# Kernel tuning notes

Hardware: AMD Instinct MI355X
Metric: run time of the kernel (lower is better)

Reference implementation:

```python
import jax, jax.numpy as jnp
import numpy as np

EPS = 1e-5
SLOPE = 0.2


def _conv(x, w, b, stride, pad):
    y = jax.lax.conv_general_dilated(
        x, w, (stride, stride), ((pad, pad), (pad, pad)),
        dimension_numbers=('NCHW', 'OIHW', 'NCHW'))
    return y + b[None, :, None, None]


def _inorm(x):
    m = x.mean(axis=(2, 3), keepdims=True)
    v = x.var(axis=(2, 3), keepdims=True)
    return (x - m) * jax.lax.rsqrt(v + EPS)


def _down(x, w, b, norm):
    y = _conv(x, w, b, 2, 1)
    if norm:
        y = _inorm(y)
    return jax.nn.leaky_relu(y, SLOPE)


def _self_attn(x, wq, bq, wk, bk, wv, bv, gamma):
    B, C, H, W = x.shape
    N = H * W
    q = _conv(x, wq, bq, 1, 0).reshape(B, -1, N)   # (B, C/8, N)
    k = _conv(x, wk, bk, 1, 0).reshape(B, -1, N)
    v = _conv(x, wv, bv, 1, 0).reshape(B, C, N)
    attn = jax.nn.softmax(jnp.einsum('bcn,bcm->bnm', q, k), axis=-1)  # (B,N,N)
    out = jnp.einsum('bcm,bnm->bcn', v, attn).reshape(B, C, H, W)
    return gamma * out + x


def _branch(p, img):
    (w0, b0, w1, b1, w2, b2, wq, bq, wk, bk, wv, bv, gamma, wh, bh) = p
    x = _down(img, w0, b0, norm=False)
    x = _down(x, w1, b1, norm=True)
    x = _self_attn(x, wq, bq, wk, bk, wv, bv, gamma)
    x = _down(x, w2, b2, norm=True)
    return _conv(x, wh, bh, 1, 1)  # head: Conv2d(nf*4, 1, 4, padding=1)


def setup_inputs() -> dict:
    key = jax.random.key(0)
    ks = jax.random.split(key, 20)
    S, B, H = 4, 16, 128
    s = 0.05  # weight scale for numerical stability of softmax energies
    d = {
        'img': jax.random.normal(ks[0], (B, 1, H, H), jnp.float32),
        'stage_idx': jax.random.randint(ks[1], (B,), 0, S, jnp.int32),
        'w0': jax.random.normal(ks[2], (S, 64, 1, 4, 4)) * s,
        'b0': jax.random.normal(ks[3], (S, 64)) * s,
        'w1': jax.random.normal(ks[4], (S, 128, 64, 4, 4)) * s,
        'b1': jax.random.normal(ks[5], (S, 128)) * s,
        'w2': jax.random.normal(ks[6], (S, 256, 128, 4, 4)) * s,
        'b2': jax.random.normal(ks[7], (S, 256)) * s,
        'wq': jax.random.normal(ks[8], (S, 16, 128, 1, 1)) * s,
        'bq': jax.random.normal(ks[9], (S, 16)) * s,
        'wk': jax.random.normal(ks[10], (S, 16, 128, 1, 1)) * s,
        'bk': jax.random.normal(ks[11], (S, 16)) * s,
        'wv': jax.random.normal(ks[12], (S, 128, 128, 1, 1)) * s,
        'bv': jax.random.normal(ks[13], (S, 128)) * s,
        'gamma': jax.random.normal(ks[14], (S,)) * s,
        'wh': jax.random.normal(ks[15], (S, 1, 256, 4, 4)) * s,
        'bh': jax.random.normal(ks[16], (S, 1)) * s,
    }
    return d


def reference(img, stage_idx, w0, b0, w1, b1, w2, b2, wq, bq, wk, bk, wv, bv, gamma, wh, bh):
    params = (w0, b0, w1, b1, w2, b2, wq, bq, wk, bk, wv, bv, gamma, wh, bh)
    # compute every branch for every sample (as the original), stacked over stage axis
    all_preds = jax.vmap(_branch, in_axes=(0, None))(params, img)  # (S, B, 1, h, w)
    B = img.shape[0]
    return all_preds[stage_idx, jnp.arange(B)]  # (B, 1, h, w)
```

## Files before the change

kernel.cpp:

```cpp
#include <hip/hip_runtime.h>

#define LRELU(x) ((x) > 0.0f ? (x) : 0.2f * (x))
#define SB __builtin_amdgcn_sched_barrier(0)

typedef short bf16x8 __attribute__((ext_vector_type(8)));
typedef short bf16x4 __attribute__((ext_vector_type(4)));
typedef float f32x4 __attribute__((ext_vector_type(4)));

__device__ __forceinline__ short f2bf(float f) {
  union { float f; unsigned u; } x{f};
  return (short)((x.u + 0x7FFF + ((x.u >> 16) & 1)) >> 16);
}

__global__ __launch_bounds__(256) void k_repack_all(
    const float* __restrict__ w1, unsigned short* __restrict__ wr1,
    const float* __restrict__ w2, unsigned short* __restrict__ wr2,
    const float* __restrict__ bh, const int* __restrict__ sidx,
    float* __restrict__ out, unsigned short* __restrict__ x0t,
    unsigned short* __restrict__ ybf, const float* __restrict__ img,
    const float* __restrict__ w0, const float* __restrict__ b0,
    float* __restrict__ stat) {
  __shared__ float Ish[4 * 34];
  if (blockIdx.x >= 2853) {
    const int t = threadIdx.x;
    const int q = blockIdx.x - 2853;
    const int b = q >> 8, py = q & 255;
    const int oh = py >> 2, owb = (py & 3) << 4;
    const int s = sidx[b];
    const float* ip = img + (size_t)b * 16384;
    if (t < 136) {
      int r = t / 34, c = t % 34;
      int ih = 2 * oh - 1 + r, iw = 2 * owb - 1 + c;
      Ish[t] = ((unsigned)ih < 128u && (unsigned)iw < 128u) ? ip[ih * 128 + iw] : 0.f;
    }
    const int co = t & 63, ps = t >> 6;
    float wreg[16];
    const float* wp = w0 + (s * 64 + co) * 16;
#pragma unroll
    for (int i = 0; i < 16; i++) wreg[i] = wp[i];
    float bb = b0[s * 64 + co];
    __syncthreads();
    unsigned short* op = x0t + ((size_t)b * 4356 + (oh + 1) * 66 + (owb + 1)) * 64 + co;
#pragma unroll
    for (int j = 0; j < 4; j++) {
      int pl = ps * 4 + j;
      float acc = bb;
#pragma unroll
      for (int kh = 0; kh < 4; kh++)
#pragma unroll
        for (int kw = 0; kw < 4; kw++)
          acc += wreg[kh * 4 + kw] * Ish[kh * 34 + pl * 2 + kw];
      acc = LRELU(acc);
      op[pl * 64] = (unsigned short)f2bf(acc);
    }
    return;
  }
  int idx = blockIdx.x * 256 + threadIdx.x;
  if (idx < 131072) {
    float4 v = *(const float4*)(w1 + (size_t)idx * 4);
    int base = idx * 4;
    int tap0 = base & 15;
    int rest = base >> 4;
    int ci = rest & 63, sco = rest >> 6;
    unsigned short* d = wr1 + (size_t)sco * 1024 + ci;
    d[(tap0 + 0) * 64] = (unsigned short)f2bf(v.x);
    d[(tap0 + 1) * 64] = (unsigned short)f2bf(v.y);
    d[(tap0 + 2) * 64] = (unsigned short)f2bf(v.z);
    d[(tap0 + 3) * 64] = (unsigned short)f2bf(v.w);
    return;
  } else if (idx < 655360) {
    int i = idx - 131072;
    float4 v = *(const float4*)(w2 + (size_t)i * 4);
    int base = i * 4;
    int tap0 = base & 15;
    int rest = base >> 4;
    int ci = rest & 127, sco = rest >> 7;
    unsigned short* d = wr2 + (size_t)sco * 2048 + ci;
    d[(tap0 + 0) * 128] = (unsigned short)f2bf(v.x);
    d[(tap0 + 1) * 128] = (unsigned short)f2bf(v.y);
    d[(tap0 + 2) * 128] = (unsigned short)f2bf(v.z);
    d[(tap0 + 3) * 128] = (unsigned short)f2bf(v.w);
    return;
  } else if (idx < 658960) {
    int i = idx - 655360;
    if (i < 3600) out[i] = bh[sidx[i / 225]];
    return;
  } else if (idx < 692240) {
    int i = idx - 658960;
    int b = i / 2080, r = i % 2080;
    int pix = r >> 3, sub = r & 7;
    int row, col;
    if (pix < 66) { row = 0; col = pix; }
    else if (pix < 132) { row = 65; col = pix - 66; }
    else { int qq = pix - 132; row = 1 + (qq >> 1); col = (qq & 1) * 65; }
    bf16x8 z = {0, 0, 0, 0, 0, 0, 0, 0};
    *(bf16x8*)(x0t + ((size_t)b * 4356 + row * 66 + col) * 64 + sub * 8) = z;
    return;
  } else if (idx < 726032) {
    int i = idx - 692240;
    if (i >= 33792) return;
    int b = i / 2112, r = i % 2112;
    int pix = r >> 4, sub = r & 15;
    int row, col;
    if (pix < 34) { row = 0; col = pix; }
    else if (pix < 68) { row = 33; col = pix - 34; }
    else { int qq = pix - 68; row = 1 + (qq >> 1); col = (qq & 1) * 33; }
    bf16x8 z = {0, 0, 0, 0, 0, 0, 0, 0};
    *(bf16x8*)(ybf + ((size_t)b * 1156 + row * 34 + col) * 128 + sub * 8) = z;
    return;
  } else {
    int i = idx - 726032;
    if (i < 4096) stat[i] = 0.f;
    return;
  }
}

__global__ __launch_bounds__(256, 2) void k_conv1n(
    const unsigned short* __restrict__ x0t, const unsigned short* __restrict__ wr,
    const int* __restrict__ sidx, float* __restrict__ x1,
    float* __restrict__ stat) {
  __shared__ __align__(16) unsigned short Xs[26624];
  const int t = threadIdx.x;
  const int c = blockIdx.x & 7, rr = blockIdx.x >> 3;
  const int b = c + 8 * (rr >> 5);
  const int y = rr & 31;
  const int ne = y & 15;
  const int cog = y >> 4;
  const int s = sidx[b];
  const int lane = t & 63, wv = t >> 6;
  const int quad = lane >> 4, l16 = lane & 15;

  const unsigned short* gb = x0t + ((size_t)b * 4356 + 4 * ne * 66) * 64;
  {
    float4 v[13];
#pragma unroll
    for (int i = 0; i < 13; i++) v[i] = *(const float4*)(gb + (i * 256 + t) * 8);
#pragma unroll
    for (int i = 0; i < 13; i++) {
      int ba = (i * 256 + t) * 16;
      int sw = ba ^ (((ba >> 9) & 7) << 4);
      *(float4*)((char*)Xs + sw) = v[i];
    }
  }
  __syncthreads();

  const int co0w = cog * 64 + wv * 16;
  const unsigned short* ap = wr + ((size_t)(s * 128 + co0w + l16)) * 1024 + quad * 8;
  f32x4 acc[4];
#pragma unroll
  for (int nt = 0; nt < 4; nt++) acc[nt] = (f32x4){0.f, 0.f, 0.f, 0.f};

#pragma unroll
  for (int kc = 0; kc < 32; kc++) {
    const int tap = kc >> 1;
    const int cio = (kc & 1) * 32 + quad * 8;
    const int kh = tap >> 2, kw = tap & 3;
    bf16x8 af = *(const bf16x8*)(ap + kc * 32);
#pragma unroll
    for (int nt = 0; nt < 4; nt++) {
      int lr = 2 * (nt >> 1) + kh;
      int col = 2 * ((nt & 1) * 16 + l16) + kw;
      int ba = ((lr * 66 + col) * 64 + cio) * 2;
      int sw = ba ^ (((ba >> 9) & 7) << 4);
      bf16x8 bv = *(const bf16x8*)((const char*)Xs + sw);
      acc[nt] = __builtin_amdgcn_mfma_f32_16x16x32_bf16(af, bv, acc[nt], 0, 0, 0);
    }
  }

#pragma unroll
  for (int r = 0; r < 4; r++) {
    float sv = acc[0][r] + acc[1][r] + acc[2][r] + acc[3][r];
    float sq = acc[0][r] * acc[0][r] + acc[1][r] * acc[1][r] +
               acc[2][r] * acc[2][r] + acc[3][r] * acc[3][r];
#pragma unroll
    for (int o = 1; o < 16; o <<= 1) {
      sv += __shfl_xor(sv, o, 64);
      sq += __shfl_xor(sq, o, 64);
    }
    if (l16 == 0) {
      int co = co0w + quad * 4 + r;
      atomicAdd(&stat[(b * 128 + co) * 2 + 0], sv);
      atomicAdd(&stat[(b * 128 + co) * 2 + 1], sq);
    }
  }

#pragma unroll
  for (int nt = 0; nt < 4; nt++) {
    int p = ne * 64 + (nt >> 1) * 32 + (nt & 1) * 16 + l16;
#pragma unroll
    for (int r = 0; r < 4; r++)
      x1[((size_t)b * 128 + co0w + quad * 4 + r) * 1024 + p] = acc[nt][r];
  }
}

__global__ __launch_bounds__(256) void k_proj_qkv(
    const float* __restrict__ xin, const float* __restrict__ wq,
    const float* __restrict__ bq, const float* __restrict__ wk,
    const float* __restrict__ bk, const float* __restrict__ wv,
    const float* __restrict__ bv, const int* __restrict__ sidx,
    const float* __restrict__ stat,
    float* __restrict__ q, float* __restrict__ kout, unsigned short* __restrict__ vpk) {
  __shared__ float xsh[32 * 256];
  __shared__ float wsh[16 * 32];
  __shared__ float msh[128], ish[128];
  const int t = threadIdx.x;
  const int c = blockIdx.x & 7, rr = blockIdx.x >> 3;
  const int half = (rr >= 40) ? 1 : 0;
  const int b = c + 8 * half;
  const int y = rr - half * 40;
  const int s = sidx[b];
  const int cg = t >> 6, ng = t & 63;
  const float* w;
  const float* bias;
  int co0, nn0, CO;
  if (y < 8) {
    w = (y < 4) ? wq : wk;
    bias = (y < 4) ? bq : bk;
    co0 = 0;
    nn0 = (y & 3) * 256;
    CO = 16;
  } else {
    w = wv;
    bias = bv;
    co0 = ((y - 8) >> 2) * 16;
    nn0 = ((y - 8) & 3) * 256;
    CO = 128;
  }
  if (t < 128) {
    float sv = stat[(b * 128 + t) * 2 + 0];
    float sq = stat[(b * 128 + t) * 2 + 1];
    float m = sv * (1.0f / 1024.0f);
    float var = sq * (1.0f / 1024.0f) - m * m;
    msh[t] = m;
    ish[t] = rsqrtf(var + 1e-5f);
  }
  const float* xb = xin + (size_t)b * 128 * 1024;
  float4 acc4[4];
#pragma unroll
  for (int cix = 0; cix < 4; cix++) {
    float bb = bias[s * CO + co0 + cg * 4 + cix];
    acc4[cix] = make_float4(bb, bb, bb, bb);
  }
  __syncthreads();
  for (int cc = 0; cc < 4; cc++) {
#pragma unroll
    for (int k = 0; k < 8; k++) {
      int id = t + (k << 8);
      int ci = id >> 6, nf = id & 63;
      float4 v = ((const float4*)(xb + (cc * 32 + ci) * 1024 + nn0))[nf];
      float m = msh[cc * 32 + ci], iv = ish[cc * 32 + ci];
      v.x = (v.x - m) * iv; v.x = LRELU(v.x);
      v.y = (v.y - m) * iv; v.y = LRELU(v.y);
      v.z = (v.z - m) * iv; v.z = LRELU(v.z);
      v.w = (v.w - m) * iv; v.w = LRELU(v.w);
      ((float4*)xsh)[id] = v;
    }
    if (t < 128)
      ((float4*)wsh)[t] =
          ((const float4*)(w + ((size_t)(s * CO + co0 + (t >> 3))) * 128 + cc * 32))[t & 7];
    __syncthreads();
#pragma unroll
    for (int ci4 = 0; ci4 < 8; ci4++) {
      float4 wvv[4], xv[4];
#pragma unroll
      for (int cix = 0; cix < 4; cix++) wvv[cix] = ((const float4*)wsh)[(cg * 4 + cix) * 8 + ci4];
#pragma unroll
      for (int i = 0; i < 4; i++) xv[i] = ((const float4*)xsh)[(ci4 * 4 + i) * 64 + ng];
#pragma unroll
      for (int cix = 0; cix < 4; cix++)
#pragma unroll
        for (int i = 0; i < 4; i++) {
          float wvc = i == 0 ? wvv[cix].x : i == 1 ? wvv[cix].y : i == 2 ? wvv[cix].z : wvv[cix].w;
          acc4[cix].x += wvc * xv[i].x;
          acc4[cix].y += wvc * xv[i].y;
          acc4[cix].z += wvc * xv[i].z;
          acc4[cix].w += wvc * xv[i].w;
        }
    }
    __syncthreads();
  }
  if (y < 8) {
    float* outp = (y < 4) ? q : kout;
#pragma unroll
    for (int cix = 0; cix < 4; cix++)
      ((float4*)(outp + ((size_t)b * 16 + cg * 4 + cix) * 1024 + nn0))[ng] = acc4[cix];
  } else {
    int n = nn0 + ng * 4;
#pragma unroll
    for (int cix = 0; cix < 4; cix++) {
      int co = co0 + cg * 4 + cix;
      bf16x4 u;
      u[0] = f2bf(acc4[cix].x);
      u[1] = f2bf(acc4[cix].y);
      u[2] = f2bf(acc4[cix].z);
      u[3] = f2bf(acc4[cix].w);
      *(bf16x4*)(vpk + (((size_t)b * 32 + (n >> 5)) * 128 + co) * 32 + (n & 31)) = u;
    }
  }
}

__global__ __launch_bounds__(256, 2) void k_attn(
    const float* __restrict__ q, const float* __restrict__ k,
    const unsigned short* __restrict__ vpk, const float* __restrict__ x1,
    const float* __restrict__ gamma, const int* __restrict__ sidx,
    const float* __restrict__ stat, unsigned short* __restrict__ ybf) {
  __shared__ __align__(16) short Psh[16 * 1032];
  __shared__ __align__(16) unsigned short Ks[16384];
  __shared__ float redm[64], reds[64];
  const int t = threadIdx.x;
  const int c = blockIdx.x & 7, rr = blockIdx.x >> 3;
  const int b = c + 8 * (rr >> 6);
  const int n0 = (rr & 63) << 4;
  const int lane = t & 63, wv = t >> 6;
  const int quad = lane >> 4, l16 = lane & 15;
  const float* qb = q + (size_t)b * 16 * 1024;
  const float* kb = k + (size_t)b * 16 * 1024;
  const float* xb = x1 + (size_t)b * 128 * 1024;

  bf16x8 qf = {0, 0, 0, 0, 0, 0, 0, 0};
  if (quad < 2) {
#pragma unroll
    for (int i = 0; i < 8; i++)
      qf[i] = f2bf(qb[(size_t)(quad * 8 + i) * 1024 + n0 + l16]);
  }

#pragma unroll
  for (int cg = 0; cg < 4; cg++) {
    float4 v0 = *(const float4*)(kb + (size_t)(cg * 4 + 0) * 1024 + 4 * t);
    float4 v1 = *(const float4*)(kb + (size_t)(cg * 4 + 1) * 1024 + 4 * t);
    float4 v2 = *(const float4*)(kb + (size_t)(cg * 4 + 2) * 1024 + 4 * t);
    float4 v3 = *(const float4*)(kb + (size_t)(cg * 4 + 3) * 1024 + 4 * t);
#pragma unroll
    for (int j = 0; j < 4; j++) {
      float a0 = j == 0 ? v0.x : j == 1 ? v0.y : j == 2 ? v0.z : v0.w;
      float a1 = j == 0 ? v1.x : j == 1 ? v1.y : j == 2 ? v1.z : v1.w;
      float a2 = j == 0 ? v2.x : j == 1 ? v2.y : j == 2 ? v2.z : v2.w;
      float a3 = j == 0 ? v3.x : j == 1 ? v3.y : j == 2 ? v3.z : v3.w;
      bf16x4 pk;
      pk[0] = f2bf(a0);
      pk[1] = f2bf(a1);
      pk[2] = f2bf(a2);
      pk[3] = f2bf(a3);
      *(bf16x4*)&Ks[(4 * t + j) * 16 + cg * 4] = pk;
    }
  }
  __syncthreads();

  f32x4 sacc[16];
#pragma unroll
  for (int tt = 0; tt < 16; tt++) sacc[tt] = (f32x4){0.f, 0.f, 0.f, 0.f};
  const int mwb = wv * 256;
#pragma unroll
  for (int tt = 0; tt < 16; tt++) {
    bf16x8 afr = {0, 0, 0, 0, 0, 0, 0, 0};
    if (quad < 2)
      afr = *(const bf16x8*)&Ks[(mwb + tt * 16 + l16) * 16 + quad * 8];
    sacc[tt] = __builtin_amdgcn_mfma_f32_16x16x32_bf16(afr, qf, sacc[tt], 0, 0, 0);
  }

  float lmax = sacc[0][0];
#pragma unroll
  for (int tt = 0; tt < 16; tt++)
#pragma unroll
    for (int r = 0; r < 4; r++) lmax = fmaxf(lmax, sacc[tt][r]);
  lmax = fmaxf(lmax, __shfl_xor(lmax, 16, 64));
  lmax = fmaxf(lmax, __shfl_xor(lmax, 32, 64));
  if (lane < 16) redm[wv * 16 + lane] = lmax;
  __syncthreads();
  float gmax = fmaxf(fmaxf(redm[l16], redm[16 + l16]), fmaxf(redm[32 + l16], redm[48 + l16]));

  float lsum = 0.f;
#pragma unroll
  for (int tt = 0; tt < 16; tt++) {
    bf16x4 pv4;
#pragma unroll
    for (int r = 0; r < 4; r++) {
      float e = __expf(sacc[tt][r] - gmax);
      lsum += e;
      pv4[r] = f2bf(e);
    }
    *(bf16x4*)&Psh[l16 * 1032 + mwb + tt * 16 + quad * 4] = pv4;
  }
  lsum += __shfl_xor(lsum, 16, 64);
  lsum += __shfl_xor(lsum, 32, 64);
  if (lane < 16) reds[wv * 16 + lane] = lsum;
  __syncthreads();

  const unsigned short* vp =
      vpk + ((size_t)b * 32 * 128 + (size_t)(wv * 32 + l16)) * 32 + quad * 8;
  const short* prow = Psh + l16 * 1032 + quad * 8;
  f32x4 dacc[2];
  dacc[0] = (f32x4){0.f, 0.f, 0.f, 0.f};
  dacc[1] = (f32x4){0.f, 0.f, 0.f, 0.f};

  bf16x8 VA0[4], VA1[4], PAr[4];
  bf16x8 VB0[4], VB1[4], PBr[4];
#define LDV(V0, V1, PR, G)                                \
  _Pragma("unroll") for (int m4 = 0; m4 < 4; m4++) {      \
    int mt = (G) * 4 + m4;                                \
    V0[m4] = *(const bf16x8*)(vp + mt * 4096);            \
    V1[m4] = *(const bf16x8*)(vp + 512 + mt * 4096);      \
    PR[m4] = *(const bf16x8*)(prow + mt * 32);            \
  }                                                       \
  SB;
#define MMV(V0, V1, PR)                                                                      \
  _Pragma("unroll") for (int m4 = 0; m4 < 4; m4++) {                                         \
    dacc[0] = __builtin_amdgcn_mfma_f32_16x16x32_bf16(V0[m4], PR[m4], dacc[0], 0, 0, 0);     \
    dacc[1] = __builtin_amdgcn_mfma_f32_16x16x32_bf16(V1[m4], PR[m4], dacc[1], 0, 0, 0);     \
  }                                                                                          \
  SB;

  LDV(VA0, VA1, PAr, 0)
  LDV(VB0, VB1, PBr, 1)
  MMV(VA0, VA1, PAr) LDV(VA0, VA1, PAr, 2)
  MMV(VB0, VB1, PBr) LDV(VB0, VB1, PBr, 3)
  MMV(VA0, VA1, PAr) LDV(VA0, VA1, PAr, 4)
  MMV(VB0, VB1, PBr) LDV(VB0, VB1, PBr, 5)
  MMV(VA0, VA1, PAr) LDV(VA0, VA1, PAr, 6)
  MMV(VB0, VB1, PBr) LDV(VB0, VB1, PBr, 7)
  MMV(VA0, VA1, PAr)
  MMV(VB0, VB1, PBr)
#undef LDV
#undef MMV
  __syncthreads();

  float* Osh = (float*)Psh;
  short* Osh2 = Psh + 4352;
#pragma unroll
  for (int i = 0; i < 2; i++) {
    int cob = wv * 32 + i * 16 + quad * 4;
#pragma unroll
    for (int r = 0; r < 4; r++) Osh[(cob + r) * 17 + l16] = dacc[i][r];
  }
  __syncthreads();
  float g = gamma[sidx[b]];
  {
    int co = t >> 1, j0 = (t & 1) * 8;
    float sv = stat[(b * 128 + co) * 2 + 0];
    float sq = stat[(b * 128 + co) * 2 + 1];
    float mm = sv * (1.0f / 1024.0f);
    float iv = rsqrtf(sq * (1.0f / 1024.0f) - mm * mm + 1e-5f);
    const float* xr = xb + (co << 10) + n0 + j0;
    float4 xv0 = *(const float4*)xr;
    float4 xv1 = *(const float4*)(xr + 4);
    float xs[8] = {xv0.x, xv0.y, xv0.z, xv0.w, xv1.x, xv1.y, xv1.z, xv1.w};
#pragma unroll
    for (int j = 0; j < 8; j++) {
      float nv = (xs[j] - mm) * iv;
      xs[j] = LRELU(nv);
    }
#pragma unroll
    for (int j = 0; j < 8; j++) {
      int nl = j0 + j;
      float rs = 1.0f / (reds[nl] + reds[16 + nl] + reds[32 + nl] + reds[48 + nl]);
      Osh2[nl * 136 + co] = f2bf(g * Osh[co * 17 + nl] * rs + xs[j]);
    }
  }
  __syncthreads();
  {
    int nl = t >> 4, cg = t & 15;
    bf16x8 u = *(const bf16x8*)&Osh2[nl * 136 + cg * 8];
    int p = n0 + nl;
    int ih = p >> 5, iw = p & 31;
    *(bf16x8*)(ybf + ((size_t)b * 1156 + (ih + 1) * 34 + (iw + 1)) * 128 + cg * 8) = u;
  }
}

__global__ __launch_bounds__(256, 2) void k_conv2n(
    const unsigned short* __restrict__ ybf, const unsigned short* __restrict__ wr,
    const int* __restrict__ sidx, float* __restrict__ x2) {
  __shared__ __align__(16) unsigned short Xs[26624];
  const int t = threadIdx.x;
  const int c = blockIdx.x & 7, rr = blockIdx.x >> 3;
  const int b = c + 8 * (rr >> 5);
  const int y = rr & 31;
  const int ne = y & 7;
  const int cog = y >> 3;
  const int s = sidx[b];
  const int lane = t & 63, wv = t >> 6;
  const int quad = lane >> 4, l16 = lane & 15;

  const unsigned short* gb = ybf + ((size_t)b * 1156 + 4 * ne * 34) * 128;
  {
    float4 v[13];
#pragma unroll
    for (int i = 0; i < 13; i++) v[i] = *(const float4*)(gb + (i * 256 + t) * 8);
#pragma unroll
    for (int i = 0; i < 13; i++) {
      int ba = (i * 256 + t) * 16;
      int sw = ba ^ (((ba >> 9) & 7) << 4);
      *(float4*)((char*)Xs + sw) = v[i];
    }
  }
  __syncthreads();

  const int co0w = cog * 64 + wv * 16;
  const unsigned short* ap = wr + ((size_t)(s * 256 + co0w + l16)) * 2048 + quad * 8;
  f32x4 acc[2];
  acc[0] = (f32x4){0.f, 0.f, 0.f, 0.f};
  acc[1] = (f32x4){0.f, 0.f, 0.f, 0.f};

#pragma unroll
  for (int kc = 0; kc < 64; kc++) {
    const int tap = kc >> 2;
    const int cio = (kc & 3) * 32 + quad * 8;
    const int kh = tap >> 2, kw = tap & 3;
    bf16x8 af = *(const bf16x8*)(ap + kc * 32);
#pragma unroll
    for (int nt = 0; nt < 2; nt++) {
      int lr = 2 * nt + kh;
      int col = 2 * l16 + kw;
      int ba = ((lr * 34 + col) * 128 + cio) * 2;
      int sw = ba ^ (((ba >> 9) & 7) << 4);
      bf16x8 bv = *(const bf16x8*)((const char*)Xs + sw);
      acc[nt] = __builtin_amdgcn_mfma_f32_16x16x32_bf16(af, bv, acc[nt], 0, 0, 0);
    }
  }

#pragma unroll
  for (int nt = 0; nt < 2; nt++) {
    int p = ne * 32 + nt * 16 + l16;
#pragma unroll
    for (int r = 0; r < 4; r++)
      x2[((size_t)b * 256 + co0w + quad * 4 + r) * 256 + p] = acc[nt][r];
  }
}

__global__ __launch_bounds__(256) void k_head_part(
    const float* __restrict__ x2, const float* __restrict__ wh,
    const int* __restrict__ sidx, float* __restrict__ out) {
  __shared__ float Xs[32 * 256];
  __shared__ float Wsh[512];
  __shared__ float sm[32], si[32];
  const int t = threadIdx.x;
  const int b = blockIdx.x, cc = blockIdx.y;
  const int s = sidx[b];
  const float* xp = x2 + ((size_t)b * 256 + cc * 32) * 256;
#pragma unroll
  for (int i = 0; i < 32; i++) Xs[i * 256 + t] = xp[i * 256 + t];
#pragma unroll
  for (int i = 0; i < 2; i++) {
    int idx = i * 256 + t;
    Wsh[idx] = wh[s * 4096 + cc * 512 + idx];
  }
  __syncthreads();
  {
    int r = t >> 3, c0 = (t & 7) * 32;
    float sv = 0.f, sq = 0.f;
#pragma unroll
    for (int j = 0; j < 32; j++) {
      float v = Xs[r * 256 + c0 + j];
      sv += v;
      sq += v * v;
    }
#pragma unroll
    for (int o = 1; o < 8; o <<= 1) {
      sv += __shfl_xor(sv, o, 64);
      sq += __shfl_xor(sq, o, 64);
    }
    if ((t & 7) == 0) {
      float m = sv * (1.0f / 256.0f);
      float var = sq * (1.0f / 256.0f) - m * m;
      sm[r] = m;
      si[r] = rsqrtf(var + 1e-5f);
    }
  }
  __syncthreads();
#pragma unroll
  for (int i = 0; i < 32; i++) {
    float v = (Xs[i * 256 + t] - sm[i]) * si[i];
    Xs[i * 256 + t] = LRELU(v);
  }
  __syncthreads();
  if (t < 225) {
    int oh = t / 15, ow = t % 15;
    float acc = 0.0f;
    for (int ci = 0; ci < 32; ci++) {
      const float* xr = Xs + ci * 256;
      const float* wr = Wsh + ci * 16;
#pragma unroll
      for (int kh = 0; kh < 4; kh++) {
        int ih = oh - 1 + kh;
        if ((unsigned)ih >= 16u) continue;
#pragma unroll
        for (int kw = 0; kw < 4; kw++) {
          int iw = ow - 1 + kw;
          if ((unsigned)iw >= 16u) continue;
          acc += wr[kh * 4 + kw] * xr[(ih << 4) + iw];
        }
      }
    }
    atomicAdd(out + b * 225 + t, acc);
  }
}

extern "C" void kernel_launch(void* const* d_in, const int* in_sizes, int n_in,
                              void* d_out, int out_size, void* d_ws, size_t ws_size,
                              hipStream_t stream) {
  const float* img = (const float*)d_in[0];
  const int* sidx = (const int*)d_in[1];
  const float* w0 = (const float*)d_in[2];
  const float* b0 = (const float*)d_in[3];
  const float* w1 = (const float*)d_in[4];
  const float* w2 = (const float*)d_in[6];
  const float* wq = (const float*)d_in[8];
  const float* bq = (const float*)d_in[9];
  const float* wk = (const float*)d_in[10];
  const float* bk = (const float*)d_in[11];
  const float* wv = (const float*)d_in[12];
  const float* bv = (const float*)d_in[13];
  const float* gamma = (const float*)d_in[14];
  const float* wh = (const float*)d_in[15];
  const float* bh = (const float*)d_in[16];
  float* out = (float*)d_out;

  float* ws = (float*)d_ws;
  unsigned short* x0t = (unsigned short*)(ws);
  float* x1 = ws + 2359296;
  float* q = ws + 4456448;
  float* k = ws + 4718592;
  unsigned short* vpk = (unsigned short*)(ws + 4980736);
  unsigned short* ybf = (unsigned short*)(ws + 6029312);
  float* x2 = ws + 7340032;
  float* stat = ws + 8650752;
  unsigned short* wr1 = (unsigned short*)(ws + 8912896);
  unsigned short* wr2 = (unsigned short*)(ws + 9175040);

  k_repack_all<<<6949, 256, 0, stream>>>(w1, wr1, w2, wr2, bh, sidx, out, x0t, ybf,
                                         img, w0, b0, stat);
  k_conv1n<<<512, 256, 0, stream>>>(x0t, wr1, sidx, x1, stat);
  k_proj_qkv<<<640, 256, 0, stream>>>(x1, wq, bq, wk, bk, wv, bv, sidx, stat, q, k, vpk);
  k_attn<<<1024, 256, 0, stream>>>(q, k, vpk, x1, gamma, sidx, stat, ybf);
  k_conv2n<<<512, 256, 0, stream>>>(ybf, wr2, sidx, x2);
  k_head_part<<<dim3(16, 8), 256, 0, stream>>>(x2, wh, sidx, out);
}
```

Before: 200.3 us.

## Emit Q/K as bf16 position-major from projection and load MFMA fragments directly

The projection kernel now writes Q and K as bf16 in a position-major [n][16] layout instead of fp32 channel-major. The attention kernel no longer loads all of K, converts it and stages it in shared memory behind a barrier. It reads MFMA fragments for Q and K straight from global memory. This halves Q/K traffic, removes the per-block conversion work and 32KB of LDS (which may allow more occupancy), but K fragments are now fetched from global or L2 rather than LDS.

Result: no change. 197.8 us (-1.2%).

```diff
diff --git a/kernel.cpp b/kernel.cpp
--- a/kernel.cpp
+++ b/kernel.cpp
@@ -199,7 +199,8 @@
     const float* __restrict__ bk, const float* __restrict__ wv,
     const float* __restrict__ bv, const int* __restrict__ sidx,
     const float* __restrict__ stat,
-    float* __restrict__ q, float* __restrict__ kout, unsigned short* __restrict__ vpk) {
+    unsigned short* __restrict__ qbf, unsigned short* __restrict__ kbf,
+    unsigned short* __restrict__ vpk) {
   __shared__ float xsh[32 * 256];
   __shared__ float wsh[16 * 32];
   __shared__ float msh[128], ish[128];
@@ -280,10 +281,18 @@
     __syncthreads();
   }
   if (y < 8) {
-    float* outp = (y < 4) ? q : kout;
-#pragma unroll
-    for (int cix = 0; cix < 4; cix++)
-      ((float4*)(outp + ((size_t)b * 16 + cg * 4 + cix) * 1024 + nn0))[ng] = acc4[cix];
+    unsigned short* outp = ((y < 4) ? qbf : kbf) + (size_t)b * 16384;
+#pragma unroll
+    for (int j = 0; j < 4; j++) {
+      bf16x4 u;
+#pragma unroll
+      for (int cix = 0; cix < 4; cix++) {
+        float v = j == 0 ? acc4[cix].x : j == 1 ? acc4[cix].y : j == 2 ? acc4[cix].z
+                                                                       : acc4[cix].w;
+        u[cix] = f2bf(v);
+      }
+      *(bf16x4*)(outp + (size_t)(nn0 + ng * 4 + j) * 16 + cg * 4) = u;
+    }
   } else {
     int n = nn0 + ng * 4;
 #pragma unroll
@@ -300,12 +309,11 @@
 }
 
 __global__ __launch_bounds__(256, 2) void k_attn(
-    const float* __restrict__ q, const float* __restrict__ k,
+    const unsigned short* __restrict__ qbf, const unsigned short* __restrict__ kbf,
     const unsigned short* __restrict__ vpk, const float* __restrict__ x1,
     const float* __restrict__ gamma, const int* __restrict__ sidx,
     const float* __restrict__ stat, unsigned short* __restrict__ ybf) {
   __shared__ __align__(16) short Psh[16 * 1032];
-  __shared__ __align__(16) unsigned short Ks[16384];
   __shared__ float redm[64], reds[64];
   const int t = threadIdx.x;
   const int c = blockIdx.x & 7, rr = blockIdx.x >> 3;
@@ -313,38 +321,12 @@
   const int n0 = (rr & 63) << 4;
   const int lane = t & 63, wv = t >> 6;
   const int quad = lane >> 4, l16 = lane & 15;
-  const float* qb = q + (size_t)b * 16 * 1024;
-  const float* kb = k + (size_t)b * 16 * 1024;
+  const unsigned short* qbb = qbf + (size_t)b * 16384;
+  const unsigned short* kbb = kbf + (size_t)b * 16384;
   const float* xb = x1 + (size_t)b * 128 * 1024;
 
   bf16x8 qf = {0, 0, 0, 0, 0, 0, 0, 0};
-  if (quad < 2) {
-#pragma unroll
-    for (int i = 0; i < 8; i++)
-      qf[i] = f2bf(qb[(size_t)(quad * 8 + i) * 1024 + n0 + l16]);
-  }
-
-#pragma unroll
-  for (int cg = 0; cg < 4; cg++) {
-    float4 v0 = *(const float4*)(kb + (size_t)(cg * 4 + 0) * 1024 + 4 * t);
-    float4 v1 = *(const float4*)(kb + (size_t)(cg * 4 + 1) * 1024 + 4 * t);
-    float4 v2 = *(const float4*)(kb + (size_t)(cg * 4 + 2) * 1024 + 4 * t);
-    float4 v3 = *(const float4*)(kb + (size_t)(cg * 4 + 3) * 1024 + 4 * t);
-#pragma unroll
-    for (int j = 0; j < 4; j++) {
-      float a0 = j == 0 ? v0.x : j == 1 ? v0.y : j == 2 ? v0.z : v0.w;
-      float a1 = j == 0 ? v1.x : j == 1 ? v1.y : j == 2 ? v1.z : v1.w;
-      float a2 = j == 0 ? v2.x : j == 1 ? v2.y : j == 2 ? v2.z : v2.w;
-      float a3 = j == 0 ? v3.x : j == 1 ? v3.y : j == 2 ? v3.z : v3.w;
-      bf16x4 pk;
-      pk[0] = f2bf(a0);
-      pk[1] = f2bf(a1);
-      pk[2] = f2bf(a2);
-      pk[3] = f2bf(a3);
-      *(bf16x4*)&Ks[(4 * t + j) * 16 + cg * 4] = pk;
-    }
-  }
-  __syncthreads();
+  if (quad < 2) qf = *(const bf16x8*)(qbb + (size_t)(n0 + l16) * 16 + quad * 8);
 
   f32x4 sacc[16];
 #pragma unroll
@@ -354,7 +336,7 @@
   for (int tt = 0; tt < 16; tt++) {
     bf16x8 afr = {0, 0, 0, 0, 0, 0, 0, 0};
     if (quad < 2)
-      afr = *(const bf16x8*)&Ks[(mwb + tt * 16 + l16) * 16 + quad * 8];
+      afr = *(const bf16x8*)(kbb + (size_t)(mwb + tt * 16 + l16) * 16 + quad * 8);
     sacc[tt] = __builtin_amdgcn_mfma_f32_16x16x32_bf16(afr, qf, sacc[tt], 0, 0, 0);
   }
 
@@ -617,8 +599,8 @@
   float* ws = (float*)d_ws;
   unsigned short* x0t = (unsigned short*)(ws);
   float* x1 = ws + 2359296;
-  float* q = ws + 4456448;
-  float* k = ws + 4718592;
+  unsigned short* qbf = (unsigned short*)(ws + 4456448);
+  unsigned short* kbf = (unsigned short*)(ws + 4718592);
   unsigned short* vpk = (unsigned short*)(ws + 4980736);
   unsigned short* ybf = (unsigned short*)(ws + 6029312);
   float* x2 = ws + 7340032;
@@ -629,8 +611,8 @@
   k_repack_all<<<6949, 256, 0, stream>>>(w1, wr1, w2, wr2, bh, sidx, out, x0t, ybf,
                                          img, w0, b0, stat);
   k_conv1n<<<512, 256, 0, stream>>>(x0t, wr1, sidx, x1, stat);
-  k_proj_qkv<<<640, 256, 0, stream>>>(x1, wq, bq, wk, bk, wv, bv, sidx, stat, q, k, vpk);
-  k_attn<<<1024, 256, 0, stream>>>(q, k, vpk, x1, gamma, sidx, stat, ybf);
+  k_proj_qkv<<<640, 256, 0, stream>>>(x1, wq, bq, wk, bk, wv, bv, sidx, stat, qbf, kbf, vpk);
+  k_attn<<<1024, 256, 0, stream>>>(qbf, kbf, vpk, x1, gamma, sidx, stat, ybf);
   k_conv2n<<<512, 256, 0, stream>>>(ybf, wr2, sidx, x2);
   k_head_part<<<dim3(16, 8), 256, 0, stream>>>(x2, wh, sidx, out);
 }
```
